# Optimization experiments

Measured on AMD Instinct MI355X. Metric: run time of the kernel, lower is better.

## Reference

```python
import jax, jax.numpy as jnp
import numpy as np
from jax import lax

GROUPS = 32
EPS = 1e-5
COMMON_STRIDE = 4


def conv3x3(x, w):
    # x: [B,C,H,W], w: [O,I,3,3], stride 1, padding 1 ('SAME'), no bias
    return lax.conv_general_dilated(x, w, (1, 1), 'SAME',
                                    dimension_numbers=('NCHW', 'OIHW', 'NCHW'))


def group_norm(x, scale, bias):
    b, c, h, w = x.shape
    xg = x.reshape(b, GROUPS, c // GROUPS, h, w)
    mean = xg.mean(axis=(2, 3, 4), keepdims=True)
    var = xg.var(axis=(2, 3, 4), keepdims=True)
    xg = (xg - mean) * lax.rsqrt(var + EPS)
    x = xg.reshape(b, c, h, w)
    return x * scale[None, :, None, None] + bias[None, :, None, None]


def head(x, w, s, bta):
    return jax.nn.relu(group_norm(conv3x3(x, w), s, bta))


def setup_inputs() -> dict:
    key = jax.random.key(0)
    ks = jax.random.split(key, 4)
    B, Cin, H, W = 2, 256, 64, 64
    Cd, K = 128, 19
    fan3 = Cin * 9
    return {
        'x': jax.random.normal(ks[0], (B, Cin, H, W), jnp.float32),
        'w_pam': jax.random.normal(ks[1], (Cd, Cin, 3, 3), jnp.float32) * np.sqrt(2.0 / fan3),
        'gn_pam_scale': jnp.ones((Cd,), jnp.float32),
        'gn_pam_bias': jnp.zeros((Cd,), jnp.float32),
        'w_cam': jax.random.normal(ks[2], (Cd, Cin, 3, 3), jnp.float32) * np.sqrt(2.0 / fan3),
        'gn_cam_scale': jnp.ones((Cd,), jnp.float32),
        'gn_cam_bias': jnp.zeros((Cd,), jnp.float32),
        'w_pred': jax.random.normal(ks[3], (K, Cd, 1, 1), jnp.float32) * np.sqrt(2.0 / Cd),
        'b_pred': jnp.zeros((K,), jnp.float32),
    }


def reference(x, w_pam, gn_pam_scale, gn_pam_bias, w_cam, gn_cam_scale, gn_cam_bias,
              w_pred, b_pred):
    pam = head(x, w_pam, gn_pam_scale, gn_pam_bias)   # [B,C,H,W]
    cam = head(x, w_cam, gn_cam_scale, gn_cam_bias)   # [B,C,H,W]
    b, c, h, w = pam.shape
    n = h * w

    # --- PAM: spatial self-attention, unscaled QK^T softmax V (Q=K=V=pam) ---
    Bm = pam.reshape(b, c, n)                                   # [B,C,N]
    pam_w = jax.nn.softmax(jnp.einsum('bci,bcj->bij', Bm, Bm), axis=-1)  # [B,N,N]
    weighted_pam = jnp.einsum('bij,bcj->bci', pam_w, Bm).reshape(b, c, h, w)
    sum_pam = pam + weighted_pam

    # --- CAM: channel self-attention over [C,C] gram matrix ---
    Am = cam.reshape(b, c, n)                                   # [B,C,N]
    cam_w = jax.nn.softmax(jnp.einsum('bcn,bdn->bcd', Am, Am), axis=-1)  # [B,C,C]
    weighted_cam = jnp.einsum('bcd,bdn->bcn', cam_w, Am).reshape(b, c, h, w)
    sum_cam = cam + weighted_cam

    # --- predictor (1x1 conv with bias) + bilinear upsample x common_stride ---
    fused = sum_pam + sum_cam
    logits = jnp.einsum('bchw,kc->bkhw', fused, w_pred[:, :, 0, 0]) + b_pred[None, :, None, None]
    out = jax.image.resize(logits, (b, logits.shape[1], h * COMMON_STRIDE, w * COMMON_STRIDE),
                           method='bilinear')  # half-pixel centers == align_corners=False
    return out
```

## Files before the change

### kernel.cpp

```cpp
#include <hip/hip_runtime.h>

#define BB 2
#define CIN 256
#define HH 64
#define WW 64
#define NPIX 4096
#define CD 128
#define CO2 256
#define KOUT 19
#define EPSV 1e-5f
#define SPAD 4356
#define KW9 2304

typedef __attribute__((ext_vector_type(8))) short bf16x8;
typedef __attribute__((ext_vector_type(4))) float f32x4;

__device__ inline unsigned short f2bf(float f) {
  unsigned u = __float_as_uint(f);
  u += 0x7fffu + ((u >> 16) & 1u);
  return (unsigned short)(u >> 16);
}
__device__ inline float bf2f(unsigned short h) {
  return __uint_as_float((unsigned)h << 16);
}
__device__ inline void f2bf_pair(float f, unsigned short& hi, unsigned short& lo) {
  hi = f2bf(f);
  const float fhi = __uint_as_float((unsigned)hi << 16);
  lo = f2bf(f - fhi);
}

__global__ __launch_bounds__(64) void zhalo_kernel(
    unsigned short* __restrict__ xThi, unsigned short* __restrict__ xTlo)
{
  const int p = blockIdx.x;
  const int b = blockIdx.y;
  int s;
  if (p < 66) s = p;
  else if (p < 132) s = 65 * 66 + (p - 66);
  else { const int q = p - 132; s = (1 + (q >> 1)) * 66 + (q & 1) * 65; }
  const size_t o = (((size_t)(b * 32 + (threadIdx.x >> 1))) * SPAD + s) * 8
                 + (threadIdx.x & 1) * 4;
  *reinterpret_cast<uint2*>(&xThi[o]) = make_uint2(0, 0);
  *reinterpret_cast<uint2*>(&xTlo[o]) = make_uint2(0, 0);
}

__global__ __launch_bounds__(256) void xpose_kernel(
    const float* __restrict__ x, unsigned short* __restrict__ xThi,
    unsigned short* __restrict__ xTlo)
{
  const int y = blockIdx.x;
  const int cig = blockIdx.y;
  const int b = blockIdx.z;
  __shared__ float Tl[32][65];
  const int t = threadIdx.x;
  {
    const int cl = t >> 3, pg = t & 7;
    const float* src = x + ((size_t)(b * CIN + cig * 32 + cl)) * NPIX + y * 64 + pg * 8;
    const float4 v0 = *reinterpret_cast<const float4*>(src);
    const float4 v1 = *reinterpret_cast<const float4*>(src + 4);
    Tl[cl][pg * 8 + 0] = v0.x; Tl[cl][pg * 8 + 1] = v0.y;
    Tl[cl][pg * 8 + 2] = v0.z; Tl[cl][pg * 8 + 3] = v0.w;
    Tl[cl][pg * 8 + 4] = v1.x; Tl[cl][pg * 8 + 5] = v1.y;
    Tl[cl][pg * 8 + 6] = v1.z; Tl[cl][pg * 8 + 7] = v1.w;
  }
  __syncthreads();
  {
    const int sl = t >> 2, cg = t & 3;
    unsigned short hh[8], ll[8];
    #pragma unroll
    for (int i = 0; i < 8; ++i) f2bf_pair(Tl[cg * 8 + i][sl], hh[i], ll[i]);
    uint4 ph, pl;
    ph.x = (unsigned)hh[0] | ((unsigned)hh[1] << 16);
    ph.y = (unsigned)hh[2] | ((unsigned)hh[3] << 16);
    ph.z = (unsigned)hh[4] | ((unsigned)hh[5] << 16);
    ph.w = (unsigned)hh[6] | ((unsigned)hh[7] << 16);
    pl.x = (unsigned)ll[0] | ((unsigned)ll[1] << 16);
    pl.y = (unsigned)ll[2] | ((unsigned)ll[3] << 16);
    pl.z = (unsigned)ll[4] | ((unsigned)ll[5] << 16);
    pl.w = (unsigned)ll[6] | ((unsigned)ll[7] << 16);
    const size_t o = (((size_t)(b * 32 + cig * 4 + cg)) * SPAD
                     + (y + 1) * 66 + 1 + sl) * 8;
    *reinterpret_cast<uint4*>(&xThi[o]) = ph;
    *reinterpret_cast<uint4*>(&xTlo[o]) = pl;
  }
}

__global__ __launch_bounds__(256) void wbconv_kernel(
    const float* __restrict__ w_pam, const float* __restrict__ w_cam,
    unsigned short* __restrict__ wbhi, unsigned short* __restrict__ wblo)
{
  const int co = blockIdx.x;
  const float* wsrc = (co < CD) ? (w_pam + (size_t)co * KW9)
                                : (w_cam + (size_t)(co - CD) * KW9);
  const int t = threadIdx.x;
  #pragma unroll
  for (int i = 0; i < 9; ++i) {
    const int idx = i * 256 + t;
    const int q = idx >> 8, ci = idx & 255;
    unsigned short h, l;
    f2bf_pair(wsrc[ci * 9 + q], h, l);
    const size_t dest = ((((size_t)(co >> 4) * 9 + q) * 8 + (ci >> 5)) * 4
                        + ((ci >> 3) & 3)) * 128 + (co & 15) * 8 + (ci & 7);
    wbhi[dest] = h;
    wblo[dest] = l;
  }
}

__global__ __launch_bounds__(256) void conv_mfma_kernel(
    const unsigned short* __restrict__ xThi, const unsigned short* __restrict__ xTlo,
    const unsigned short* __restrict__ wbhi, const unsigned short* __restrict__ wblo,
    float* __restrict__ out)
{
  const int pxt = blockIdx.x;
  const int cot = blockIdx.y;
  const int b = blockIdx.z;
  const int tid = threadIdx.x;
  const int w = tid >> 6;
  const int lane = tid & 63;
  const int m = lane & 15, g = lane >> 4;
  const int p0 = pxt * 64;
  const int y = p0 >> 6;
  const int sbase = (y + 1) * 66 + 1;

  __shared__ float Obuf[4][64][68];

  f32x4 acc[4][4];
  #pragma unroll
  for (int mt = 0; mt < 4; ++mt)
    #pragma unroll
    for (int jg = 0; jg < 4; ++jg)
      #pragma unroll
      for (int r = 0; r < 4; ++r) acc[mt][jg][r] = 0.f;

  for (int q = 0; q < 9; ++q) {
    const int dq = (q / 3 - 1) * 66 + (q % 3 - 1);
    #pragma unroll
    for (int kk2 = 0; kk2 < 2; ++kk2) {
      const int kkc = w * 2 + kk2;
      const size_t cb = (((size_t)(b * 32 + kkc * 4 + g)) * SPAD + sbase + dq + m) * 8;
      bf16x8 bh[4], bl[4];
      #pragma unroll
      for (int jg = 0; jg < 4; ++jg) {
        bh[jg] = *reinterpret_cast<const bf16x8*>(&xThi[cb + (size_t)(jg * 16) * 8]);
        bl[jg] = *reinterpret_cast<const bf16x8*>(&xTlo[cb + (size_t)(jg * 16) * 8]);
      }
      #pragma unroll
      for (int mt = 0; mt < 4; ++mt) {
        const size_t wbase = ((((size_t)(cot * 4 + mt) * 9 + q) * 8 + kkc) * 4 + g) * 128
                             + m * 8;
        const bf16x8 ah = *reinterpret_cast<const bf16x8*>(&wbhi[wbase]);
        const bf16x8 al = *reinterpret_cast<const bf16x8*>(&wblo[wbase]);
        #pragma unroll
        for (int jg = 0; jg < 4; ++jg) {
          acc[mt][jg] = __builtin_amdgcn_mfma_f32_16x16x32_bf16(ah, bh[jg], acc[mt][jg], 0, 0, 0);
          acc[mt][jg] = __builtin_amdgcn_mfma_f32_16x16x32_bf16(ah, bl[jg], acc[mt][jg], 0, 0, 0);
          acc[mt][jg] = __builtin_amdgcn_mfma_f32_16x16x32_bf16(al, bh[jg], acc[mt][jg], 0, 0, 0);
        }
      }
    }
  }

  #pragma unroll
  for (int mt = 0; mt < 4; ++mt)
    #pragma unroll
    for (int jg = 0; jg < 4; ++jg)
      #pragma unroll
      for (int r = 0; r < 4; ++r)
        Obuf[w][mt * 16 + g * 4 + r][jg * 16 + m] = acc[mt][jg][r];
  __syncthreads();

  const int co_l = tid >> 2;
  const int pxq = (tid & 3) * 16;
  float* op = out + ((size_t)b * CO2 + cot * 64 + co_l) * NPIX + p0 + pxq;
  #pragma unroll
  for (int i = 0; i < 4; ++i) {
    float4 s;
    s.x = Obuf[0][co_l][pxq + i * 4 + 0] + Obuf[1][co_l][pxq + i * 4 + 0]
        + Obuf[2][co_l][pxq + i * 4 + 0] + Obuf[3][co_l][pxq + i * 4 + 0];
    s.y = Obuf[0][co_l][pxq + i * 4 + 1] + Obuf[1][co_l][pxq + i * 4 + 1]
        + Obuf[2][co_l][pxq + i * 4 + 1] + Obuf[3][co_l][pxq + i * 4 + 1];
    s.z = Obuf[0][co_l][pxq + i * 4 + 2] + Obuf[1][co_l][pxq + i * 4 + 2]
        + Obuf[2][co_l][pxq + i * 4 + 2] + Obuf[3][co_l][pxq + i * 4 + 2];
    s.w = Obuf[0][co_l][pxq + i * 4 + 3] + Obuf[1][co_l][pxq + i * 4 + 3]
        + Obuf[2][co_l][pxq + i * 4 + 3] + Obuf[3][co_l][pxq + i * 4 + 3];
    *reinterpret_cast<float4*>(&op[i * 4]) = s;
  }
}

__global__ __launch_bounds__(256) void gn_stats_kernel(
    const float* __restrict__ conv, float* __restrict__ meanb, float* __restrict__ rstdb)
{
  const int g = blockIdx.x;
  const float* base = conv + (size_t)g * (4 * NPIX);
  float s = 0.f, ss = 0.f;
  const float4* b4 = reinterpret_cast<const float4*>(base);
  for (int i = threadIdx.x; i < 4096; i += 256) {
    float4 v = b4[i];
    s += v.x + v.y + v.z + v.w;
    ss += v.x * v.x + v.y * v.y + v.z * v.z + v.w * v.w;
  }
  #pragma unroll
  for (int off = 32; off > 0; off >>= 1) {
    s += __shfl_down(s, off);
    ss += __shfl_down(ss, off);
  }
  __shared__ float rs[4], rss[4];
  const int lane = threadIdx.x & 63, wv = threadIdx.x >> 6;
  if (lane == 0) { rs[wv] = s; rss[wv] = ss; }
  __syncthreads();
  if (threadIdx.x == 0) {
    const float S = rs[0] + rs[1] + rs[2] + rs[3];
    const float SS = rss[0] + rss[1] + rss[2] + rss[3];
    const float inv = 1.f / 16384.f;
    const float m = S * inv;
    const float var = SS * inv - m * m;
    meanb[g] = m;
    rstdb[g] = rsqrtf(var + EPSV);
  }
}

__global__ __launch_bounds__(256) void gn_pack_kernel(
    float* __restrict__ conv, const float* __restrict__ meanb, const float* __restrict__ rstdb,
    const float* __restrict__ sc_pam, const float* __restrict__ bi_pam,
    const float* __restrict__ sc_cam, const float* __restrict__ bi_cam,
    unsigned short* __restrict__ Kf2, unsigned short* __restrict__ Vf2,
    unsigned short* __restrict__ Cfhi, unsigned short* __restrict__ Cflo)
{
  const int px0 = blockIdx.x * 64;
  const int c0  = blockIdx.y * 32;
  const int b   = blockIdx.z;
  __shared__ float Tl[32][72];
  const int t = threadIdx.x;
  {
    const int cl = t >> 3, pg = t & 7;
    const int c = c0 + cl;
    const int gi = (b * 256 + c) >> 2;
    const int head = c >> 7, cc = c & 127;
    const float mean = meanb[gi], rstd = rstdb[gi];
    const float sc = head ? sc_cam[cc] : sc_pam[cc];
    const float bi = head ? bi_cam[cc] : bi_pam[cc];
    float* src = conv + ((size_t)b * CO2 + c) * NPIX + px0 + pg * 8;
    float4 v0 = *reinterpret_cast<const float4*>(src);
    float4 v1 = *reinterpret_cast<const float4*>(src + 4);
    v0.x = fmaxf((v0.x - mean) * rstd * sc + bi, 0.f);
    v0.y = fmaxf((v0.y - mean) * rstd * sc + bi, 0.f);
    v0.z = fmaxf((v0.z - mean) * rstd * sc + bi, 0.f);
    v0.w = fmaxf((v0.w - mean) * rstd * sc + bi, 0.f);
    v1.x = fmaxf((v1.x - mean) * rstd * sc + bi, 0.f);
    v1.y = fmaxf((v1.y - mean) * rstd * sc + bi, 0.f);
    v1.z = fmaxf((v1.z - mean) * rstd * sc + bi, 0.f);
    v1.w = fmaxf((v1.w - mean) * rstd * sc + bi, 0.f);
    *reinterpret_cast<float4*>(src) = v0;
    *reinterpret_cast<float4*>(src + 4) = v1;
    Tl[cl][pg * 8 + 0] = v0.x; Tl[cl][pg * 8 + 1] = v0.y;
    Tl[cl][pg * 8 + 2] = v0.z; Tl[cl][pg * 8 + 3] = v0.w;
    Tl[cl][pg * 8 + 4] = v1.x; Tl[cl][pg * 8 + 5] = v1.y;
    Tl[cl][pg * 8 + 6] = v1.z; Tl[cl][pg * 8 + 7] = v1.w;
  }
  __syncthreads();
  if (c0 < CD) {
    unsigned short* Kb = Kf2 + (size_t)b * 524288;
    unsigned short* Vb = Vf2 + (size_t)b * 524288;
    {
      const int jblk_l = t >> 6, rem = t & 63;
      const int gk = rem >> 4, mk = rem & 15;
      const int jblk = (px0 >> 4) + jblk_l;
      const int kk = c0 >> 5;
      unsigned short h[8];
      #pragma unroll
      for (int e = 0; e < 8; ++e) h[e] = f2bf(Tl[gk * 8 + e][jblk_l * 16 + mk]);
      uint4 packed;
      packed.x = (unsigned)h[0] | ((unsigned)h[1] << 16);
      packed.y = (unsigned)h[2] | ((unsigned)h[3] << 16);
      packed.z = (unsigned)h[4] | ((unsigned)h[5] << 16);
      packed.w = (unsigned)h[6] | ((unsigned)h[7] << 16);
      *reinterpret_cast<uint4*>(&Kb[(size_t)(jblk * 16 + kk * 4 + gk) * 128 + mk * 8]) = packed;
    }
    {
      const int ct_l = t >> 7, kt = (t >> 6) & 1, gv = (t >> 4) & 3, mv = t & 15;
      const int ct = (c0 >> 4) + ct_l;
      const int jc = px0 >> 6;
      unsigned short h[8];
      #pragma unroll
      for (int e = 0; e < 8; ++e) h[e] = f2bf(Tl[ct_l * 16 + mv][kt * 32 + gv * 8 + e]);
      uint4 packed;
      packed.x = (unsigned)h[0] | ((unsigned)h[1] << 16);
      packed.y = (unsigned)h[2] | ((unsigned)h[3] << 16);
      packed.z = (unsigned)h[4] | ((unsigned)h[5] << 16);
      packed.w = (unsigned)h[6] | ((unsigned)h[7] << 16);
      *reinterpret_cast<uint4*>(
          &Vb[(size_t)(((ct * 64 + jc) * 2 + kt) * 4 + gv) * 128 + mv * 8]) = packed;
    }
  } else {
    const int ct_l = t >> 7, kk_l = (t >> 6) & 1, gc = (t >> 4) & 3, mc = t & 15;
    const int ctg = ((c0 - CD) >> 4) + ct_l;
    const int kkg = (px0 >> 5) + kk_l;
    unsigned short hh[8], ll[8];
    #pragma unroll
    for (int e = 0; e < 8; ++e)
      f2bf_pair(Tl[ct_l * 16 + mc][kk_l * 32 + gc * 8 + e], hh[e], ll[e]);
    uint4 ph, pl;
    ph.x = (unsigned)hh[0] | ((unsigned)hh[1] << 16);
    ph.y = (unsigned)hh[2] | ((unsigned)hh[3] << 16);
    ph.z = (unsigned)hh[4] | ((unsigned)hh[5] << 16);
    ph.w = (unsigned)hh[6] | ((unsigned)hh[7] << 16);
    pl.x = (unsigned)ll[0] | ((unsigned)ll[1] << 16);
    pl.y = (unsigned)ll[2] | ((unsigned)ll[3] << 16);
    pl.z = (unsigned)ll[4] | ((unsigned)ll[5] << 16);
    pl.w = (unsigned)ll[6] | ((unsigned)ll[7] << 16);
    const size_t o = (((size_t)(b * 128 + kkg) * 8 + ctg) * 4 + gc) * 128 + mc * 8;
    *reinterpret_cast<uint4*>(&Cfhi[o]) = ph;
    *reinterpret_cast<uint4*>(&Cflo[o]) = pl;
  }
}

__global__ __launch_bounds__(512) void cam_gram_mfma_kernel(
    const unsigned short* __restrict__ Cfhi, const unsigned short* __restrict__ Cflo,
    float* __restrict__ gpart8)
{
  const int dt = blockIdx.x;
  const int b = blockIdx.y;
  const int kg = blockIdx.z;
  const int tid = threadIdx.x;
  const int w = tid >> 6;
  const int lane = tid & 63;
  const int m = lane & 15, g = lane >> 4;

  __shared__ float Gbuf[4][128][17];

  f32x4 acc[8];
  #pragma unroll
  for (int ct = 0; ct < 8; ++ct)
    #pragma unroll
    for (int r = 0; r < 4; ++r) acc[ct][r] = 0.f;

  const int kk = kg * 8 + w;
  const size_t base = (size_t)(b * 128 + kk) * 8;
  const bf16x8 dh = *reinterpret_cast<const bf16x8*>(&Cfhi[((base + dt) * 4 + g) * 128 + m * 8]);
  const bf16x8 dl = *reinterpret_cast<const bf16x8*>(&Cflo[((base + dt) * 4 + g) * 128 + m * 8]);
  #pragma unroll
  for (int ct = 0; ct < 8; ++ct) {
    const bf16x8 ah = *reinterpret_cast<const bf16x8*>(&Cfhi[((base + ct) * 4 + g) * 128 + m * 8]);
    const bf16x8 al = *reinterpret_cast<const bf16x8*>(&Cflo[((base + ct) * 4 + g) * 128 + m * 8]);
    acc[ct] = __builtin_amdgcn_mfma_f32_16x16x32_bf16(ah, dh, acc[ct], 0, 0, 0);
    acc[ct] = __builtin_amdgcn_mfma_f32_16x16x32_bf16(ah, dl, acc[ct], 0, 0, 0);
    acc[ct] = __builtin_amdgcn_mfma_f32_16x16x32_bf16(al, dh, acc[ct], 0, 0, 0);
  }

  if (w < 4) {
    #pragma unroll
    for (int ct = 0; ct < 8; ++ct)
      #pragma unroll
      for (int r = 0; r < 4; ++r)
        Gbuf[w][ct * 16 + g * 4 + r][m] = acc[ct][r];
  }
  __syncthreads();
  if (w >= 4) {
    #pragma unroll
    for (int ct = 0; ct < 8; ++ct)
      #pragma unroll
      for (int r = 0; r < 4; ++r)
        Gbuf[w - 4][ct * 16 + g * 4 + r][m] += acc[ct][r];
  }
  __syncthreads();
  const int c = tid >> 2;
  const int d0 = (tid & 3) * 4;
  float* gp = gpart8 + (((size_t)(kg * BB + b) * 128 + c)) * 128 + dt * 16;
  #pragma unroll
  for (int j = 0; j < 4; ++j) {
    const int d = d0 + j;
    gp[d] = Gbuf[0][c][d] + Gbuf[1][c][d] + Gbuf[2][c][d] + Gbuf[3][c][d];
  }
}

__global__ __launch_bounds__(128) void cam_softmax_kernel(
    const float* __restrict__ gpart8, float* __restrict__ camw)
{
  const int bc = blockIdx.x;
  const int b = bc >> 7, c = bc & 127;
  const int d = threadIdx.x;
  float g = 0.f;
  #pragma unroll
  for (int s = 0; s < 16; ++s)
    g += gpart8[(((size_t)(s * BB + b) * 128 + c)) * 128 + d];
  float m = g;
  #pragma unroll
  for (int off = 32; off > 0; off >>= 1) m = fmaxf(m, __shfl_xor(m, off));
  __shared__ float sm[2], ssum[2];
  const int lane = d & 63, wv = d >> 6;
  if (lane == 0) sm[wv] = m;
  __syncthreads();
  m = fmaxf(sm[0], sm[1]);
  const float e = __expf(g - m);
  float s = e;
  #pragma unroll
  for (int off = 32; off > 0; off >>= 1) s += __shfl_xor(s, off);
  if (lane == 0) ssum[wv] = s;
  __syncthreads();
  camw[(size_t)bc * CD + d] = e / (ssum[0] + ssum[1]);
}

__global__ __launch_bounds__(256) void cam_apply_kernel(
    const float* __restrict__ conv, const float* __restrict__ camw, float* __restrict__ scam)
{
  const int b = blockIdx.z;
  const int c0 = blockIdx.y * 4;
  const int n = blockIdx.x * 1024 + threadIdx.x;
  const float* Am = conv + ((size_t)b * CO2 + CD) * NPIX;
  const float* Wr = camw + ((size_t)b * CD + c0) * CD;
  float acc[4][4];
  #pragma unroll
  for (int i = 0; i < 4; ++i)
    #pragma unroll
    for (int k = 0; k < 4; ++k) acc[i][k] = 0.f;
  for (int d = 0; d < CD; ++d) {
    const float w0 = Wr[d], w1 = Wr[CD + d], w2 = Wr[2 * CD + d], w3 = Wr[3 * CD + d];
    #pragma unroll
    for (int k = 0; k < 4; ++k) {
      const float a = Am[(size_t)d * NPIX + n + k * 256];
      acc[0][k] += w0 * a; acc[1][k] += w1 * a;
      acc[2][k] += w2 * a; acc[3][k] += w3 * a;
    }
  }
  #pragma unroll
  for (int i = 0; i < 4; ++i)
    #pragma unroll
    for (int k = 0; k < 4; ++k)
      scam[((size_t)b * CD + c0 + i) * NPIX + n + k * 256] =
          Am[(size_t)(c0 + i) * NPIX + n + k * 256] + acc[i][k];
}

__global__ __launch_bounds__(512) void pam_mfma_kernel(
    const unsigned short* __restrict__ Kf2, const unsigned short* __restrict__ Vf2,
    unsigned short* __restrict__ Opart, float* __restrict__ mpart,
    float* __restrict__ lpart)
{
  const int tile = blockIdx.x;
  const int b = blockIdx.y;
  const int kg = blockIdx.z;
  const int q0 = tile * 32;
  const int tid = threadIdx.x;
  const int w = tid >> 6;
  const int lane = tid & 63;
  const int m = lane & 15, g = lane >> 4;

  __shared__ __align__(16) unsigned short Sl[8][32 * 72];
  __shared__ unsigned short Obuf[4][32][130];
  __shared__ float mlm[8][32], mll[8][32], mst[32], ltt[32];

  const unsigned short* Kb = Kf2 + (size_t)b * 524288;
  const unsigned short* Vb = Vf2 + (size_t)b * 524288;

  bf16x8 qf[2][4];
  #pragma unroll
  for (int s = 0; s < 2; ++s)
    #pragma unroll
    for (int kk = 0; kk < 4; ++kk)
      qf[s][kk] = *reinterpret_cast<const bf16x8*>(
          &Kb[(size_t)(((q0 >> 4) + s) * 16 + kk * 4 + g) * 128 + m * 8]);

  f32x4 oacc[2][8];
  #pragma unroll
  for (int s = 0; s < 2; ++s)
    #pragma unroll
    for (int ct = 0; ct < 8; ++ct)
      #pragma unroll
      for (int r = 0; r < 4; ++r) oacc[s][ct][r] = 0.f;

  float mrow[2][4], lrow[2][4];
  #pragma unroll
  for (int s = 0; s < 2; ++s)
    #pragma unroll
    for (int r = 0; r < 4; ++r) { mrow[s][r] = -1e30f; lrow[s][r] = 0.f; }

  for (int t = kg * 32 + w * 4; t < kg * 32 + w * 4 + 4; ++t) {
    f32x4 sacc[2][4];
    #pragma unroll
    for (int s = 0; s < 2; ++s)
      #pragma unroll
      for (int jt = 0; jt < 4; ++jt)
        #pragma unroll
        for (int r = 0; r < 4; ++r) sacc[s][jt][r] = 0.f;
    #pragma unroll
    for (int jt = 0; jt < 4; ++jt) {
      #pragma unroll
      for (int kk = 0; kk < 4; ++kk) {
        const bf16x8 kf = *reinterpret_cast<const bf16x8*>(
            &Kb[(size_t)((t * 4 + jt) * 16 + kk * 4 + g) * 128 + m * 8]);
        sacc[0][jt] = __builtin_amdgcn_mfma_f32_16x16x32_bf16(qf[0][kk], kf, sacc[0][jt], 0, 0, 0);
        sacc[1][jt] = __builtin_amdgcn_mfma_f32_16x16x32_bf16(qf[1][kk], kf, sacc[1][jt], 0, 0, 0);
      }
    }
    float facq[2];
    #pragma unroll
    for (int s = 0; s < 2; ++s) {
      float fac[4];
      #pragma unroll
      for (int r = 0; r < 4; ++r) {
        float v = fmaxf(fmaxf(sacc[s][0][r], sacc[s][1][r]), fmaxf(sacc[s][2][r], sacc[s][3][r]));
        v = fmaxf(v, __shfl_xor(v, 1));
        v = fmaxf(v, __shfl_xor(v, 2));
        v = fmaxf(v, __shfl_xor(v, 4));
        v = fmaxf(v, __shfl_xor(v, 8));
        const float mn = fmaxf(mrow[s][r], v);
        fac[r] = __expf(fmaxf(mrow[s][r] - mn, -80.f));
        mrow[s][r] = mn;
      }
      #pragma unroll
      for (int r = 0; r < 4; ++r) {
        float ls = 0.f;
        #pragma unroll
        for (int jt = 0; jt < 4; ++jt) {
          const float e = __expf(sacc[s][jt][r] - mrow[s][r]);
          ls += e;
          Sl[w][(s * 16 + g * 4 + r) * 72 + jt * 16 + m] = f2bf(e);
        }
        ls += __shfl_xor(ls, 1);
        ls += __shfl_xor(ls, 2);
        ls += __shfl_xor(ls, 4);
        ls += __shfl_xor(ls, 8);
        lrow[s][r] = lrow[s][r] * fac[r] + ls;
      }
      const int sel = m & 3;
      const float fsel = (sel == 0) ? fac[0] : (sel == 1) ? fac[1] : (sel == 2) ? fac[2] : fac[3];
      facq[s] = __shfl(fsel, ((m >> 2) << 4) | sel);
    }
    #pragma unroll
    for (int s = 0; s < 2; ++s)
      #pragma unroll
      for (int ct = 0; ct < 8; ++ct)
        #pragma unroll
        for (int r = 0; r < 4; ++r) oacc[s][ct][r] *= facq[s];
    bf16x8 pf[2][2];
    #pragma unroll
    for (int s = 0; s < 2; ++s)
      #pragma unroll
      for (int kt = 0; kt < 2; ++kt)
        pf[s][kt] = *reinterpret_cast<const bf16x8*>(&Sl[w][(s * 16 + m) * 72 + kt * 32 + g * 8]);
    #pragma unroll
    for (int ct = 0; ct < 8; ++ct) {
      #pragma unroll
      for (int kt = 0; kt < 2; ++kt) {
        const bf16x8 vf = *reinterpret_cast<const bf16x8*>(
            &Vb[(size_t)(((ct * 64 + t) * 2 + kt) * 4 + g) * 128 + m * 8]);
        oacc[0][ct] = __builtin_amdgcn_mfma_f32_16x16x32_bf16(vf, pf[0][kt], oacc[0][ct], 0, 0, 0);
        oacc[1][ct] = __builtin_amdgcn_mfma_f32_16x16x32_bf16(vf, pf[1][kt], oacc[1][ct], 0, 0, 0);
      }
    }
  }

  float mq[2], lq[2];
  #pragma unroll
  for (int s = 0; s < 2; ++s) {
    const int sel = m & 3;
    const float msel_ = (sel == 0) ? mrow[s][0] : (sel == 1) ? mrow[s][1]
                       : (sel == 2) ? mrow[s][2] : mrow[s][3];
    mq[s] = __shfl(msel_, ((m >> 2) << 4) | sel);
    const float lsel_ = (sel == 0) ? lrow[s][0] : (sel == 1) ? lrow[s][1]
                       : (sel == 2) ? lrow[s][2] : lrow[s][3];
    lq[s] = __shfl(lsel_, ((m >> 2) << 4) | sel);
  }
  if (g == 0) {
    #pragma unroll
    for (int s = 0; s < 2; ++s) { mlm[w][s * 16 + m] = mq[s]; mll[w][s * 16 + m] = lq[s]; }
  }
  __syncthreads();
  float rsw[2];
  #pragma unroll
  for (int s = 0; s < 2; ++s) {
    const int row = s * 16 + m;
    float ms = mlm[0][row];
    #pragma unroll
    for (int sw = 1; sw < 8; ++sw) ms = fmaxf(ms, mlm[sw][row]);
    rsw[s] = __expf(fmaxf(mq[s] - ms, -80.f));
  }
  if (w < 4) {
    #pragma unroll
    for (int s = 0; s < 2; ++s)
      #pragma unroll
      for (int ct = 0; ct < 8; ++ct)
        #pragma unroll
        for (int r = 0; r < 4; ++r)
          Obuf[w][s * 16 + m][ct * 16 + g * 4 + r] = f2bf(oacc[s][ct][r] * rsw[s]);
  }
  if (w == 0 && g == 0) {
    #pragma unroll
    for (int s = 0; s < 2; ++s) {
      const int row = s * 16 + m;
      float ms = mlm[0][row];
      #pragma unroll
      for (int sw = 1; sw < 8; ++sw) ms = fmaxf(ms, mlm[sw][row]);
      float lt = 0.f;
      #pragma unroll
      for (int sw = 0; sw < 8; ++sw)
        lt += mll[sw][row] * __expf(fmaxf(mlm[sw][row] - ms, -80.f));
      mst[row] = ms;
      ltt[row] = lt;
    }
  }
  __syncthreads();
  if (w >= 4) {
    #pragma unroll
    for (int s = 0; s < 2; ++s)
      #pragma unroll
      for (int ct = 0; ct < 8; ++ct)
        #pragma unroll
        for (int r = 0; r < 4; ++r) {
          unsigned short* pp = &Obuf[w - 4][s * 16 + m][ct * 16 + g * 4 + r];
          *pp = f2bf(bf2f(*pp) + oacc[s][ct][r] * rsw[s]);
        }
  }
  __syncthreads();
  const size_t pbase = ((size_t)(kg * BB + b) * 128 + tile) * 32;
  unsigned short* Op = Opart + pbase * 128;
  const int c = tid >> 2;
  const int qh = (tid & 3) * 8;
  #pragma unroll
  for (int qq = 0; qq < 8; ++qq) {
    const int row = qh + qq;
    float o = 0.f;
    #pragma unroll
    for (int sw = 0; sw < 4; ++sw) o += bf2f(Obuf[sw][row][c]);
    Op[(size_t)row * 128 + c] = f2bf(o);
  }
  if (tid < 32) {
    mpart[pbase + tid] = mst[tid];
    lpart[pbase + tid] = ltt[tid];
  }
}

__global__ __launch_bounds__(256) void pam_merge_kernel(
    const float* __restrict__ conv, const unsigned short* __restrict__ Opart,
    const float* __restrict__ mpart, const float* __restrict__ lpart,
    float* __restrict__ spam)
{
  const int tile = blockIdx.x;
  const int b = blockIdx.y;
  const int tid = threadIdx.x;
  const int c = tid & 127;
  const int rg = tid >> 7;
  const size_t i0 = ((size_t)(0 * BB + b) * 128 + tile) * 32;
  const size_t i1 = ((size_t)(1 * BB + b) * 128 + tile) * 32;
  #pragma unroll
  for (int rr = 0; rr < 16; ++rr) {
    const int row = rg * 16 + rr;
    const float m0 = mpart[i0 + row], m1 = mpart[i1 + row];
    const float ms = fmaxf(m0, m1);
    const float w0 = __expf(fmaxf(m0 - ms, -80.f));
    const float w1 = __expf(fmaxf(m1 - ms, -80.f));
    const float l = lpart[i0 + row] * w0 + lpart[i1 + row] * w1;
    const float o = bf2f(Opart[(i0 + row) * 128 + c]) * w0
                  + bf2f(Opart[(i1 + row) * 128 + c]) * w1;
    const int q = tile * 32 + row;
    spam[((size_t)b * CD + c) * NPIX + q] =
        conv[((size_t)b * CO2 + c) * NPIX + q] + o / l;
  }
}

__global__ __launch_bounds__(256) void pred_part_kernel(
    const float* __restrict__ spam, const float* __restrict__ scam,
    const float* __restrict__ wpred, float* __restrict__ psum)
{
  const int p = blockIdx.x * 256 + threadIdx.x;
  const int slice = blockIdx.y;
  const int b = blockIdx.z;
  float acc[KOUT];
  #pragma unroll
  for (int k = 0; k < KOUT; ++k) acc[k] = 0.f;
  const float* sp = spam + (size_t)b * CD * NPIX + p;
  const float* sc = scam + (size_t)b * CD * NPIX + p;
  #pragma unroll
  for (int ci = 0; ci < 16; ++ci) {
    const int c = slice * 16 + ci;
    const float f = sp[(size_t)c * NPIX] + sc[(size_t)c * NPIX];
    #pragma unroll
    for (int k = 0; k < KOUT; ++k)
      acc[k] += f * wpred[k * CD + c];
  }
  #pragma unroll
  for (int k = 0; k < KOUT; ++k)
    psum[(((size_t)slice * BB + b) * KOUT + k) * NPIX + p] = acc[k];
}

__global__ __launch_bounds__(256) void pred_reduce_kernel(
    const float* __restrict__ psum, const float* __restrict__ bpred,
    float* __restrict__ logit)
{
  const int p = blockIdx.x * 256 + threadIdx.x;
  const int b = blockIdx.y;
  #pragma unroll
  for (int k = 0; k < KOUT; ++k) {
    float s = bpred[k];
    #pragma unroll
    for (int sl = 0; sl < 8; ++sl)
      s += psum[(((size_t)sl * BB + b) * KOUT + k) * NPIX + p];
    logit[((size_t)b * KOUT + k) * NPIX + p] = s;
  }
}

__global__ __launch_bounds__(256) void upsample_kernel(
    const float* __restrict__ logit, float* __restrict__ out)
{
  const int idx = blockIdx.x * 256 + threadIdx.x;
  if (idx >= BB * KOUT * 256 * 256) return;
  const int ox = idx & 255;
  const int oy = (idx >> 8) & 255;
  const int plane = idx >> 16;
  const float* src = logit + (size_t)plane * NPIX;
  const float sy = (oy + 0.5f) * 0.25f - 0.5f;
  const float sx = (ox + 0.5f) * 0.25f - 0.5f;
  const float fyf = floorf(sy), fxf = floorf(sx);
  const float wy = sy - fyf, wx = sx - fxf;
  const int y0 = (int)fyf, x0 = (int)fxf;
  const int y0c = y0 < 0 ? 0 : y0;
  const int y1c = (y0 + 1 > 63) ? 63 : y0 + 1;
  const int x0c = x0 < 0 ? 0 : x0;
  const int x1c = (x0 + 1 > 63) ? 63 : x0 + 1;
  const float v00 = src[y0c * 64 + x0c], v01 = src[y0c * 64 + x1c];
  const float v10 = src[y1c * 64 + x0c], v11 = src[y1c * 64 + x1c];
  const float top = v00 + (v01 - v00) * wx;
  const float bot = v10 + (v11 - v10) * wx;
  out[idx] = top + (bot - top) * wy;
}

extern "C" void kernel_launch(void* const* d_in, const int* in_sizes, int n_in,
                              void* d_out, int out_size, void* d_ws, size_t ws_size,
                              hipStream_t stream) {
  (void)in_sizes; (void)n_in; (void)out_size; (void)ws_size;
  const float* x      = (const float*)d_in[0];
  const float* w_pam  = (const float*)d_in[1];
  const float* s_pam  = (const float*)d_in[2];
  const float* b_pam  = (const float*)d_in[3];
  const float* w_cam  = (const float*)d_in[4];
  const float* s_cam  = (const float*)d_in[5];
  const float* b_cam  = (const float*)d_in[6];
  const float* w_pred = (const float*)d_in[7];
  const float* b_pred = (const float*)d_in[8];
  float* out_f = (float*)d_out;
  float* ws0 = (float*)d_ws;

  float* conv  = ws0;
  unsigned short* xThi = (unsigned short*)(ws0 + 2097152);
  unsigned short* xTlo = xThi + (size_t)BB * 32 * SPAD * 8;
  unsigned short* wbhi = (unsigned short*)(ws0 + 4327424);
  unsigned short* wblo = wbhi + (size_t)CO2 * KW9;
  unsigned short* Cfhi = (unsigned short*)(ws0 + 3145728);
  unsigned short* Cflo = (unsigned short*)(ws0 + 3670016);
  unsigned short* Opart = (unsigned short*)(ws0 + 3145728);
  float* psum  = ws0 + 3145728;
  float* mpart = ws0 + 4194304;
  float* lpart = ws0 + 4227072;
  float* gpart8 = ws0 + 4292608;
  float* camw  = ws0 + 4950016;
  float* meanb = ws0 + 4982784;
  float* rstdb = ws0 + 4982912;
  float* logit = ws0 + 4983040;

  unsigned short* Kf2 = xThi;
  unsigned short* Vf2 = Kf2 + 1048576;

  float* spam = out_f;
  float* scam = out_f + 1048576;

  zhalo_kernel<<<dim3(260, 2), 64, 0, stream>>>(xThi, xTlo);
  xpose_kernel<<<dim3(64, 8, 2), 256, 0, stream>>>(x, xThi, xTlo);
  wbconv_kernel<<<256, 256, 0, stream>>>(w_pam, w_cam, wbhi, wblo);
  conv_mfma_kernel<<<dim3(64, 4, 2), 256, 0, stream>>>(xThi, xTlo, wbhi, wblo, conv);
  gn_stats_kernel<<<128, 256, 0, stream>>>(conv, meanb, rstdb);
  gn_pack_kernel<<<dim3(64, 8, 2), 256, 0, stream>>>(conv, meanb, rstdb,
      s_pam, b_pam, s_cam, b_cam, Kf2, Vf2, Cfhi, Cflo);
  cam_gram_mfma_kernel<<<dim3(8, 2, 16), 512, 0, stream>>>(Cfhi, Cflo, gpart8);
  cam_softmax_kernel<<<256, 128, 0, stream>>>(gpart8, camw);
  cam_apply_kernel<<<dim3(4, 32, 2), 256, 0, stream>>>(conv, camw, scam);
  pam_mfma_kernel<<<dim3(128, 2, 2), 512, 0, stream>>>(Kf2, Vf2, Opart, mpart, lpart);
  pam_merge_kernel<<<dim3(128, 2), 256, 0, stream>>>(conv, Opart, mpart, lpart, spam);
  pred_part_kernel<<<dim3(16, 8, 2), 256, 0, stream>>>(spam, scam, w_pred, psum);
  pred_reduce_kernel<<<dim3(16, 2), 256, 0, stream>>>(psum, b_pred, logit);
  upsample_kernel<<<9728, 256, 0, stream>>>(logit, out_f);
}
```

Measured before the change: 204.1 us.

## Halve PAM query tile to 16 rows, share LDS buffer, raise occupancy

The PAM flash-attention kernel now processes 16 query rows per block instead of 32, doubling the grid to 256 tiles. It drops the per-query-subtile register arrays, reuses one shared buffer for both the probability tiles and the cross-wave output reduction, and adds a min-blocks launch bound. The merge kernel and partial-buffer indexing are updated to match. The aim is more resident waves and less LDS per block, in exchange for reading the K and V tiles twice as often and halving the MFMA reuse of each loaded K/V fragment.

```diff
diff --git a/kernel.cpp b/kernel.cpp
--- a/kernel.cpp
+++ b/kernel.cpp
@@ -430,7 +430,7 @@
           Am[(size_t)(c0 + i) * NPIX + n + k * 256] + acc[i][k];
 }
 
-__global__ __launch_bounds__(512) void pam_mfma_kernel(
+__global__ __launch_bounds__(512, 6) void pam_mfma_kernel(
     const unsigned short* __restrict__ Kf2, const unsigned short* __restrict__ Vf2,
     unsigned short* __restrict__ Opart, float* __restrict__ mpart,
     float* __restrict__ lpart)
@@ -438,192 +438,152 @@
   const int tile = blockIdx.x;
   const int b = blockIdx.y;
   const int kg = blockIdx.z;
-  const int q0 = tile * 32;
   const int tid = threadIdx.x;
   const int w = tid >> 6;
   const int lane = tid & 63;
   const int m = lane & 15, g = lane >> 4;
 
-  __shared__ __align__(16) unsigned short Sl[8][32 * 72];
-  __shared__ unsigned short Obuf[4][32][130];
-  __shared__ float mlm[8][32], mll[8][32], mst[32], ltt[32];
+  __shared__ __align__(16) unsigned short Sbuf[8 * 16 * 72];
+  __shared__ float mlm[8][16], mll[8][16], mst[16], ltt[16];
 
   const unsigned short* Kb = Kf2 + (size_t)b * 524288;
   const unsigned short* Vb = Vf2 + (size_t)b * 524288;
 
-  bf16x8 qf[2][4];
-  #pragma unroll
-  for (int s = 0; s < 2; ++s)
-    #pragma unroll
-    for (int kk = 0; kk < 4; ++kk)
-      qf[s][kk] = *reinterpret_cast<const bf16x8*>(
-          &Kb[(size_t)(((q0 >> 4) + s) * 16 + kk * 4 + g) * 128 + m * 8]);
-
-  f32x4 oacc[2][8];
-  #pragma unroll
-  for (int s = 0; s < 2; ++s)
-    #pragma unroll
-    for (int ct = 0; ct < 8; ++ct)
-      #pragma unroll
-      for (int r = 0; r < 4; ++r) oacc[s][ct][r] = 0.f;
-
-  float mrow[2][4], lrow[2][4];
-  #pragma unroll
-  for (int s = 0; s < 2; ++s)
-    #pragma unroll
-    for (int r = 0; r < 4; ++r) { mrow[s][r] = -1e30f; lrow[s][r] = 0.f; }
+  bf16x8 qf[4];
+  #pragma unroll
+  for (int kk = 0; kk < 4; ++kk)
+    qf[kk] = *reinterpret_cast<const bf16x8*>(
+        &Kb[(size_t)(tile * 16 + kk * 4 + g) * 128 + m * 8]);
+
+  f32x4 oacc[8];
+  #pragma unroll
+  for (int ct = 0; ct < 8; ++ct)
+    #pragma unroll
+    for (int r = 0; r < 4; ++r) oacc[ct][r] = 0.f;
+
+  float mrow[4], lrow[4];
+  #pragma unroll
+  for (int r = 0; r < 4; ++r) { mrow[r] = -1e30f; lrow[r] = 0.f; }
 
   for (int t = kg * 32 + w * 4; t < kg * 32 + w * 4 + 4; ++t) {
-    f32x4 sacc[2][4];
-    #pragma unroll
-    for (int s = 0; s < 2; ++s)
-      #pragma unroll
-      for (int jt = 0; jt < 4; ++jt)
-        #pragma unroll
-        for (int r = 0; r < 4; ++r) sacc[s][jt][r] = 0.f;
+    f32x4 sacc[4];
+    #pragma unroll
+    for (int jt = 0; jt < 4; ++jt)
+      #pragma unroll
+      for (int r = 0; r < 4; ++r) sacc[jt][r] = 0.f;
     #pragma unroll
     for (int jt = 0; jt < 4; ++jt) {
       #pragma unroll
       for (int kk = 0; kk < 4; ++kk) {
         const bf16x8 kf = *reinterpret_cast<const bf16x8*>(
             &Kb[(size_t)((t * 4 + jt) * 16 + kk * 4 + g) * 128 + m * 8]);
-        sacc[0][jt] = __builtin_amdgcn_mfma_f32_16x16x32_bf16(qf[0][kk], kf, sacc[0][jt], 0, 0, 0);
-        sacc[1][jt] = __builtin_amdgcn_mfma_f32_16x16x32_bf16(qf[1][kk], kf, sacc[1][jt], 0, 0, 0);
+        sacc[jt] = __builtin_amdgcn_mfma_f32_16x16x32_bf16(qf[kk], kf, sacc[jt], 0, 0, 0);
       }
     }
-    float facq[2];
-    #pragma unroll
-    for (int s = 0; s < 2; ++s) {
-      float fac[4];
-      #pragma unroll
-      for (int r = 0; r < 4; ++r) {
-        float v = fmaxf(fmaxf(sacc[s][0][r], sacc[s][1][r]), fmaxf(sacc[s][2][r], sacc[s][3][r]));
-        v = fmaxf(v, __shfl_xor(v, 1));
-        v = fmaxf(v, __shfl_xor(v, 2));
-        v = fmaxf(v, __shfl_xor(v, 4));
-        v = fmaxf(v, __shfl_xor(v, 8));
-        const float mn = fmaxf(mrow[s][r], v);
-        fac[r] = __expf(fmaxf(mrow[s][r] - mn, -80.f));
-        mrow[s][r] = mn;
+    float fac[4];
+    #pragma unroll
+    for (int r = 0; r < 4; ++r) {
+      float v = fmaxf(fmaxf(sacc[0][r], sacc[1][r]), fmaxf(sacc[2][r], sacc[3][r]));
+      v = fmaxf(v, __shfl_xor(v, 1));
+      v = fmaxf(v, __shfl_xor(v, 2));
+      v = fmaxf(v, __shfl_xor(v, 4));
+      v = fmaxf(v, __shfl_xor(v, 8));
+      const float mn = fmaxf(mrow[r], v);
+      fac[r] = __expf(fmaxf(mrow[r] - mn, -80.f));
+      mrow[r] = mn;
+    }
+    #pragma unroll
+    for (int r = 0; r < 4; ++r) {
+      float ls = 0.f;
+      #pragma unroll
+      for (int jt = 0; jt < 4; ++jt) {
+        const float e = __expf(sacc[jt][r] - mrow[r]);
+        ls += e;
+        Sbuf[w * 1152 + (g * 4 + r) * 72 + jt * 16 + m] = f2bf(e);
       }
-      #pragma unroll
-      for (int r = 0; r < 4; ++r) {
-        float ls = 0.f;
-        #pragma unroll
-        for (int jt = 0; jt < 4; ++jt) {
-          const float e = __expf(sacc[s][jt][r] - mrow[s][r]);
-          ls += e;
-          Sl[w][(s * 16 + g * 4 + r) * 72 + jt * 16 + m] = f2bf(e);
-        }
-        ls += __shfl_xor(ls, 1);
-        ls += __shfl_xor(ls, 2);
-        ls += __shfl_xor(ls, 4);
-        ls += __shfl_xor(ls, 8);
-        lrow[s][r] = lrow[s][r] * fac[r] + ls;
-      }
-      const int sel = m & 3;
-      const float fsel = (sel == 0) ? fac[0] : (sel == 1) ? fac[1] : (sel == 2) ? fac[2] : fac[3];
-      facq[s] = __shfl(fsel, ((m >> 2) << 4) | sel);
+      ls += __shfl_xor(ls, 1);
+      ls += __shfl_xor(ls, 2);
+      ls += __shfl_xor(ls, 4);
+      ls += __shfl_xor(ls, 8);
+      lrow[r] = lrow[r] * fac[r] + ls;
     }
-    #pragma unroll
-    for (int s = 0; s < 2; ++s)
-      #pragma unroll
-      for (int ct = 0; ct < 8; ++ct)
-        #pragma unroll
-        for (int r = 0; r < 4; ++r) oacc[s][ct][r] *= facq[s];
-    bf16x8 pf[2][2];
-    #pragma unroll
-    for (int s = 0; s < 2; ++s)
-      #pragma unroll
-      for (int kt = 0; kt < 2; ++kt)
-        pf[s][kt] = *reinterpret_cast<const bf16x8*>(&Sl[w][(s * 16 + m) * 72 + kt * 32 + g * 8]);
+    const int sel = m & 3;
+    const float fsel = (sel == 0) ? fac[0] : (sel == 1) ? fac[1] : (sel == 2) ? fac[2] : fac[3];
+    const float facq = __shfl(fsel, ((m >> 2) << 4) | sel);
+    #pragma unroll
+    for (int ct = 0; ct < 8; ++ct)
+      #pragma unroll
+      for (int r = 0; r < 4; ++r) oacc[ct][r] *= facq;
+    bf16x8 pf[2];
+    #pragma unroll
+    for (int kt = 0; kt < 2; ++kt)
+      pf[kt] = *reinterpret_cast<const bf16x8*>(&Sbuf[w * 1152 + m * 72 + kt * 32 + g * 8]);
     #pragma unroll
     for (int ct = 0; ct < 8; ++ct) {
       #pragma unroll
       for (int kt = 0; kt < 2; ++kt) {
         const bf16x8 vf = *reinterpret_cast<const bf16x8*>(
             &Vb[(size_t)(((ct * 64 + t) * 2 + kt) * 4 + g) * 128 + m * 8]);
-        oacc[0][ct] = __builtin_amdgcn_mfma_f32_16x16x32_bf16(vf, pf[0][kt], oacc[0][ct], 0, 0, 0);
-        oacc[1][ct] = __builtin_amdgcn_mfma_f32_16x16x32_bf16(vf, pf[1][kt], oacc[1][ct], 0, 0, 0);
+        oacc[ct] = __builtin_amdgcn_mfma_f32_16x16x32_bf16(vf, pf[kt], oacc[ct], 0, 0, 0);
       }
     }
   }
 
-  float mq[2], lq[2];
-  #pragma unroll
-  for (int s = 0; s < 2; ++s) {
-    const int sel = m & 3;
-    const float msel_ = (sel == 0) ? mrow[s][0] : (sel == 1) ? mrow[s][1]
-                       : (sel == 2) ? mrow[s][2] : mrow[s][3];
-    mq[s] = __shfl(msel_, ((m >> 2) << 4) | sel);
-    const float lsel_ = (sel == 0) ? lrow[s][0] : (sel == 1) ? lrow[s][1]
-                       : (sel == 2) ? lrow[s][2] : lrow[s][3];
-    lq[s] = __shfl(lsel_, ((m >> 2) << 4) | sel);
-  }
-  if (g == 0) {
-    #pragma unroll
-    for (int s = 0; s < 2; ++s) { mlm[w][s * 16 + m] = mq[s]; mll[w][s * 16 + m] = lq[s]; }
-  }
-  __syncthreads();
-  float rsw[2];
-  #pragma unroll
-  for (int s = 0; s < 2; ++s) {
-    const int row = s * 16 + m;
-    float ms = mlm[0][row];
-    #pragma unroll
-    for (int sw = 1; sw < 8; ++sw) ms = fmaxf(ms, mlm[sw][row]);
-    rsw[s] = __expf(fmaxf(mq[s] - ms, -80.f));
-  }
+  const int sel = m & 3;
+  const float msel_ = (sel == 0) ? mrow[0] : (sel == 1) ? mrow[1]
+                     : (sel == 2) ? mrow[2] : mrow[3];
+  const float mq = __shfl(msel_, ((m >> 2) << 4) | sel);
+  const float lsel_ = (sel == 0) ? lrow[0] : (sel == 1) ? lrow[1]
+                     : (sel == 2) ? lrow[2] : lrow[3];
+  const float lq = __shfl(lsel_, ((m >> 2) << 4) | sel);
+  if (g == 0) { mlm[w][m] = mq; mll[w][m] = lq; }
+  __syncthreads();
+  float ms = mlm[0][m];
+  #pragma unroll
+  for (int sw = 1; sw < 8; ++sw) ms = fmaxf(ms, mlm[sw][m]);
+  const float rsw = __expf(fmaxf(mq - ms, -80.f));
   if (w < 4) {
     #pragma unroll
-    for (int s = 0; s < 2; ++s)
-      #pragma unroll
-      for (int ct = 0; ct < 8; ++ct)
-        #pragma unroll
-        for (int r = 0; r < 4; ++r)
-          Obuf[w][s * 16 + m][ct * 16 + g * 4 + r] = f2bf(oacc[s][ct][r] * rsw[s]);
+    for (int ct = 0; ct < 8; ++ct)
+      #pragma unroll
+      for (int r = 0; r < 4; ++r)
+        Sbuf[w * 2080 + m * 130 + ct * 16 + g * 4 + r] = f2bf(oacc[ct][r] * rsw);
   }
   if (w == 0 && g == 0) {
-    #pragma unroll
-    for (int s = 0; s < 2; ++s) {
-      const int row = s * 16 + m;
-      float ms = mlm[0][row];
-      #pragma unroll
-      for (int sw = 1; sw < 8; ++sw) ms = fmaxf(ms, mlm[sw][row]);
-      float lt = 0.f;
-      #pragma unroll
-      for (int sw = 0; sw < 8; ++sw)
-        lt += mll[sw][row] * __expf(fmaxf(mlm[sw][row] - ms, -80.f));
-      mst[row] = ms;
-      ltt[row] = lt;
-    }
+    float ms2 = mlm[0][m];
+    #pragma unroll
+    for (int sw = 1; sw < 8; ++sw) ms2 = fmaxf(ms2, mlm[sw][m]);
+    float lt = 0.f;
+    #pragma unroll
+    for (int sw = 0; sw < 8; ++sw)
+      lt += mll[sw][m] * __expf(fmaxf(mlm[sw][m] - ms2, -80.f));
+    mst[m] = ms2;
+    ltt[m] = lt;
   }
   __syncthreads();
   if (w >= 4) {
     #pragma unroll
-    for (int s = 0; s < 2; ++s)
-      #pragma unroll
-      for (int ct = 0; ct < 8; ++ct)
-        #pragma unroll
-        for (int r = 0; r < 4; ++r) {
-          unsigned short* pp = &Obuf[w - 4][s * 16 + m][ct * 16 + g * 4 + r];
-          *pp = f2bf(bf2f(*pp) + oacc[s][ct][r] * rsw[s]);
-        }
-  }
-  __syncthreads();
-  const size_t pbase = ((size_t)(kg * BB + b) * 128 + tile) * 32;
+    for (int ct = 0; ct < 8; ++ct)
+      #pragma unroll
+      for (int r = 0; r < 4; ++r) {
+        unsigned short* pp = &Sbuf[(w - 4) * 2080 + m * 130 + ct * 16 + g * 4 + r];
+        *pp = f2bf(bf2f(*pp) + oacc[ct][r] * rsw);
+      }
+  }
+  __syncthreads();
+  const size_t pbase = ((size_t)(kg * BB + b) * 256 + tile) * 16;
   unsigned short* Op = Opart + pbase * 128;
   const int c = tid >> 2;
-  const int qh = (tid & 3) * 8;
-  #pragma unroll
-  for (int qq = 0; qq < 8; ++qq) {
+  const int qh = (tid & 3) * 4;
+  #pragma unroll
+  for (int qq = 0; qq < 4; ++qq) {
     const int row = qh + qq;
     float o = 0.f;
     #pragma unroll
-    for (int sw = 0; sw < 4; ++sw) o += bf2f(Obuf[sw][row][c]);
+    for (int sw = 0; sw < 4; ++sw) o += bf2f(Sbuf[sw * 2080 + row * 130 + c]);
     Op[(size_t)row * 128 + c] = f2bf(o);
   }
-  if (tid < 32) {
+  if (tid < 16) {
     mpart[pbase + tid] = mst[tid];
     lpart[pbase + tid] = ltt[tid];
   }
@@ -639,11 +599,11 @@
   const int tid = threadIdx.x;
   const int c = tid & 127;
   const int rg = tid >> 7;
-  const size_t i0 = ((size_t)(0 * BB + b) * 128 + tile) * 32;
-  const size_t i1 = ((size_t)(1 * BB + b) * 128 + tile) * 32;
-  #pragma unroll
-  for (int rr = 0; rr < 16; ++rr) {
-    const int row = rg * 16 + rr;
+  const size_t i0 = ((size_t)(0 * BB + b) * 256 + tile) * 16;
+  const size_t i1 = ((size_t)(1 * BB + b) * 256 + tile) * 16;
+  #pragma unroll
+  for (int rr = 0; rr < 8; ++rr) {
+    const int row = rg * 8 + rr;
     const float m0 = mpart[i0 + row], m1 = mpart[i1 + row];
     const float ms = fmaxf(m0, m1);
     const float w0 = __expf(fmaxf(m0 - ms, -80.f));
@@ -651,7 +611,7 @@
     const float l = lpart[i0 + row] * w0 + lpart[i1 + row] * w1;
     const float o = bf2f(Opart[(i0 + row) * 128 + c]) * w0
                   + bf2f(Opart[(i1 + row) * 128 + c]) * w1;
-    const int q = tile * 32 + row;
+    const int q = tile * 16 + row;
     spam[((size_t)b * CD + c) * NPIX + q] =
         conv[((size_t)b * CO2 + c) * NPIX + q] + o / l;
   }
@@ -772,8 +732,8 @@
   cam_gram_mfma_kernel<<<dim3(8, 2, 16), 512, 0, stream>>>(Cfhi, Cflo, gpart8);
   cam_softmax_kernel<<<256, 128, 0, stream>>>(gpart8, camw);
   cam_apply_kernel<<<dim3(4, 32, 2), 256, 0, stream>>>(conv, camw, scam);
-  pam_mfma_kernel<<<dim3(128, 2, 2), 512, 0, stream>>>(Kf2, Vf2, Opart, mpart, lpart);
-  pam_merge_kernel<<<dim3(128, 2), 256, 0, stream>>>(conv, Opart, mpart, lpart, spam);
+  pam_mfma_kernel<<<dim3(256, 2, 2), 512, 0, stream>>>(Kf2, Vf2, Opart, mpart, lpart);
+  pam_merge_kernel<<<dim3(256, 2), 256, 0, stream>>>(conv, Opart, mpart, lpart, spam);
   pred_part_kernel<<<dim3(16, 8, 2), 256, 0, stream>>>(spam, scam, w_pred, psum);
   pred_reduce_kernel<<<dim3(16, 2), 256, 0, stream>>>(psum, b_pred, logit);
   upsample_kernel<<<9728, 256, 0, stream>>>(logit, out_f);
```

Result: slower. 271.9 us (+33.2%).
